# Kernel tuning notes

Measured on AMD Instinct MI355X. Metric: run time of the kernel, lower is better.

Reference implementation:

```python
import jax, jax.numpy as jnp
import numpy as np

N = 14        # nodes per graph (fixed by hidden*14 in the Linear)
H = 4         # attention heads
F_IN = 128    # num_feature
C = 64        # hidden (per-head out_channels; concat=False -> mean over heads)
NEG_SLOPE = 0.2  # PyG GATConv default negative_slope


def gat_conv(x, src, dst, W, a_src, a_dst, b):
    """One PyG-style GATConv on a single graph.
    x: [N, F]  W: [F, H*C]  a_src/a_dst: [H, C]  b: [C]
    src/dst: [E] int (self-loops already appended). concat=False -> mean over heads.
    """
    h = (x @ W).reshape(N, H, C)                       # [N,H,C]
    al_src = jnp.einsum('nhc,hc->nh', h, a_src)        # [N,H]
    al_dst = jnp.einsum('nhc,hc->nh', h, a_dst)        # [N,H]
    e = jax.nn.leaky_relu(al_src[src] + al_dst[dst], NEG_SLOPE)  # [E,H]
    # softmax over incoming edges of each destination node (stable)
    m = jax.ops.segment_max(e, dst, num_segments=N)    # [N,H]
    ex = jnp.exp(e - m[dst])
    denom = jax.ops.segment_sum(ex, dst, num_segments=N)
    alpha = ex / denom[dst]                            # [E,H]
    out = jax.ops.segment_sum(alpha[:, :, None] * h[src], dst, num_segments=N)  # [N,H,C]
    return out.mean(axis=1) + b                        # [N,C]


def setup_inputs() -> dict:
    key = jax.random.key(0)
    ks = jax.random.split(key, 12)
    B, E = 16384, 182
    feature = jax.random.normal(ks[0], (B, N, F_IN), dtype=jnp.float32)
    edge_list = jax.random.randint(ks[1], (B, E, 2), 0, N, dtype=jnp.int64)

    def glorot(k, shape):
        fan = shape[0] + shape[-1]
        return jax.random.normal(k, shape, dtype=jnp.float32) * jnp.sqrt(2.0 / fan)

    return {
        'feature': feature,
        'edge_list': edge_list,
        'W1': glorot(ks[2], (F_IN, H * C)),
        'a_src1': glorot(ks[3], (H, C)),
        'a_dst1': glorot(ks[4], (H, C)),
        'b1': jnp.zeros((C,), jnp.float32),
        'W2': glorot(ks[5], (C, H * C)),
        'a_src2': glorot(ks[6], (H, C)),
        'a_dst2': glorot(ks[7], (H, C)),
        'b2': jnp.zeros((C,), jnp.float32),
        'W_lin': glorot(ks[8], (N * C, C // 2)),
        'b_lin': jnp.zeros((C // 2,), jnp.float32),
        'W_pred': glorot(ks[9], (C // 2, 1)),
        'b_pred': jnp.zeros((1,), jnp.float32),
    }


def reference(feature, edge_list, W1, a_src1, a_dst1, b1, W2, a_src2, a_dst2, b2,
              W_lin, b_lin, W_pred, b_pred):
    B = feature.shape[0]
    # PyG GATConv adds self-loops by default
    loops = jnp.broadcast_to(jnp.arange(N, dtype=edge_list.dtype), (B, N))
    src = jnp.concatenate([edge_list[..., 0], loops], axis=1)  # [B, E+N]
    dst = jnp.concatenate([edge_list[..., 1], loops], axis=1)

    def per_graph(x, s, d):
        h = jax.nn.relu(gat_conv(x, s, d, W1, a_src1, a_dst1, b1))
        # dropout is identity in eval mode
        h = gat_conv(h, s, d, W2, a_src2, a_dst2, b2)       # [N,C]
        z = h.reshape(-1) @ W_lin + b_lin                    # [C//2]
        p = z @ W_pred + b_pred                              # [1]
        return jax.nn.sigmoid(p)

    return jax.vmap(per_graph)(feature, src, dst)            # [B,1]
```

## Files before the change

kernel.cpp:

```cpp
#include <hip/hip_runtime.h>

#define NN 14
#define EE 182

typedef __attribute__((ext_vector_type(8))) short bf16x8;
typedef __attribute__((ext_vector_type(4))) short bf16x4;
typedef __attribute__((ext_vector_type(4))) float f32x4;
typedef __attribute__((ext_vector_type(4))) unsigned u32x4;
typedef __attribute__((ext_vector_type(2))) unsigned u32x2;

__device__ __forceinline__ unsigned f2bf(float f) {
    unsigned u = __float_as_uint(f);
    return (u + 0x7fffu + ((u >> 16) & 1u)) >> 16;
}
__device__ __forceinline__ unsigned pack2bf(float lo, float hi) {
    return __builtin_amdgcn_perm(__float_as_uint(hi) + 0x8000u,
                                 __float_as_uint(lo) + 0x8000u, 0x07060302u);
}
__device__ __forceinline__ bf16x8 mk8(unsigned a, unsigned b, unsigned c, unsigned d) {
    u32x4 u = {a, b, c, d};
    return __builtin_bit_cast(bf16x8, u);
}
__device__ __forceinline__ bf16x4 mk4(unsigned a, unsigned b) {
    u32x2 u = {a, b};
    return __builtin_bit_cast(bf16x4, u);
}

__global__ void prep_pack(const float* __restrict__ W1, const float* __restrict__ W2,
                          const float* __restrict__ Wl, const float* __restrict__ Wpred,
                          const float* __restrict__ bl, const float* __restrict__ bp,
                          const float* __restrict__ as1, const float* __restrict__ ad1,
                          const float* __restrict__ as2, const float* __restrict__ ad2,
                          short* __restrict__ wp1, short* __restrict__ wp2,
                          short* __restrict__ battn1, short* __restrict__ battn2,
                          float* __restrict__ wcombP) {
    int gid = blockIdx.x * 256 + threadIdx.x;
    if (gid < 32768) {
        int j = gid & 7, L = (gid >> 3) & 63, kk = (gid >> 9) & 3, nt = gid >> 11;
        int k = kk * 32 + (L >> 4) * 8 + j, n = nt * 16 + (L & 15);
        wp1[gid] = (short)f2bf(W1[k * 256 + n]);
    } else if (gid < 49152) {
        int g2 = gid - 32768;
        int j = g2 & 7, L = (g2 >> 3) & 63, kk = (g2 >> 9) & 1, nt = g2 >> 10;
        int k = kk * 32 + (L >> 4) * 8 + j, n = nt * 16 + (L & 15);
        wp2[g2] = (short)f2bf(W2[k * 256 + n]);
    } else if (gid < 51200) {
        int g2 = gid - 49152;
        int j = g2 & 7, L = (g2 >> 3) & 63, kk = g2 >> 9;
        int n = L & 15, k = kk * 32 + (L >> 4) * 8 + j;
        float val = 0.f;
        if (n < 8) {
            const float* av = ((n >> 2) ? ad1 : as1) + (n & 3) * 64;
            const float* wr = W1 + k * 256 + (n & 3) * 64;
            for (int c = 0; c < 64; ++c) val += wr[c] * av[c];
        }
        battn1[g2] = (short)f2bf(val);
    } else if (gid < 52224) {
        int g2 = gid - 51200;
        int j = g2 & 7, L = (g2 >> 3) & 63, kk = g2 >> 9;
        int n = L & 15, k = kk * 32 + (L >> 4) * 8 + j;
        float val = 0.f;
        if (n < 8) {
            const float* av = ((n >> 2) ? ad2 : as2) + (n & 3) * 64;
            const float* wr = W2 + k * 256 + (n & 3) * 64;
            for (int c = 0; c < 64; ++c) val += wr[c] * av[c];
        }
        battn2[g2] = (short)f2bf(val);
    } else if (gid < 56320) {
        int o = gid - 52224;
        int r = o & 3, i4 = o >> 2;
        int m = i4 & 15, ctq = i4 >> 4;
        int q = ctq & 3, ct = ctq >> 2;
        int chan = ct * 16 + q * 4 + r;
        float acc = 0.f;
        if (m < NN) {
            const float* wr = Wl + (m * 64 + chan) * 32;
            #pragma unroll
            for (int j = 0; j < 32; ++j) acc += wr[j] * Wpred[j];
        }
        wcombP[o] = acc;
    } else if (gid == 56320) {
        float acc = bp[0];
        #pragma unroll
        for (int j = 0; j < 32; ++j) acc += bl[j] * Wpred[j];
        wcombP[4096] = acc;
    }
}

template<int KK, bool RELU>
__device__ __forceinline__ void gat_layer(int lane,
    const bf16x8* a, const short* wpB,
    const float* __restrict__ bias,
    const float* cntf, const float* alsd,
    f32x4* o, unsigned (*po)[2])
{
    const int m = lane & 15, q = lane >> 4;
    f32x4 agg[4];
    #pragma unroll
    for (int ct = 0; ct < 4; ++ct) agg[ct] = f32x4{0.f, 0.f, 0.f, 0.f};

    #pragma unroll
    for (int h = 0; h < 4; ++h) {
        unsigned hf[4][2];
        #pragma unroll
        for (int ct = 0; ct < 4; ++ct) {
            f32x4 c = f32x4{0.f, 0.f, 0.f, 0.f};
            #pragma unroll
            for (int kk = 0; kk < KK; ++kk) {
                bf16x8 b = *(const bf16x8*)(wpB +
                    (((h * 4 + ct) * KK + kk) * 64 + lane) * 8);
                c = __builtin_amdgcn_mfma_f32_16x16x32_bf16(a[kk], b, c, 0, 0, 0);
            }
            hf[ct][0] = pack2bf(c[0], c[1]);
            hf[ct][1] = pack2bf(c[2], c[3]);
        }

        f32x4 alv = *(const f32x4*)(alsd + h * 16 + q * 4);
        float ad  = alsd[64 + h * 16 + m];
        f32x4 cv  = *(const f32x4*)(cntf + m * 20 + q * 4);
        float v0, v1, v2, v3;
        {
            float l0 = alv[0] + ad, l1 = alv[1] + ad, l2 = alv[2] + ad, l3 = alv[3] + ad;
            l0 = fmaxf(l0, 0.f) + 0.2f * fminf(l0, 0.f);
            l1 = fmaxf(l1, 0.f) + 0.2f * fminf(l1, 0.f);
            l2 = fmaxf(l2, 0.f) + 0.2f * fminf(l2, 0.f);
            l3 = fmaxf(l3, 0.f) + 0.2f * fminf(l3, 0.f);
            v0 = __expf(l0) * cv[0]; v1 = __expf(l1) * cv[1];
            v2 = __expf(l2) * cv[2]; v3 = __expf(l3) * cv[3];
        }
        float s = v0 + v1 + v2 + v3;
        s += __shfl_xor(s, 16);
        s += __shfl_xor(s, 32);
        float inv = (s > 0.f) ? 0.25f / s : 0.f;
        bf16x4 P = mk4(pack2bf(v0 * inv, v1 * inv), pack2bf(v2 * inv, v3 * inv));

        #pragma unroll
        for (int ct = 0; ct < 4; ++ct)
            agg[ct] = __builtin_amdgcn_mfma_f32_16x16x16bf16_1k(
                mk4(hf[ct][0], hf[ct][1]), P, agg[ct], 0, 0, 0);
    }

    #pragma unroll
    for (int ct = 0; ct < 4; ++ct) {
        float4 bb = *(const float4*)(bias + ct * 16 + q * 4);
        float o0 = agg[ct][0] + bb.x, o1 = agg[ct][1] + bb.y;
        float o2 = agg[ct][2] + bb.z, o3 = agg[ct][3] + bb.w;
        if (RELU) {
            o0 = fmaxf(o0, 0.f); o1 = fmaxf(o1, 0.f);
            o2 = fmaxf(o2, 0.f); o3 = fmaxf(o3, 0.f);
            if (m >= NN) { o0 = 0.f; o1 = 0.f; o2 = 0.f; o3 = 0.f; }
            po[ct][0] = pack2bf(o0, o1);
            po[ct][1] = pack2bf(o2, o3);
        } else {
            o[ct] = f32x4{o0, o1, o2, o3};
        }
    }
}

__global__ __launch_bounds__(1024, 4) void gat_fused(
    const float* __restrict__ feature,
    const int*   __restrict__ edge_list,
    const float* __restrict__ b1, const float* __restrict__ b2,
    const short* __restrict__ wpck,
    const float* __restrict__ wcombP,
    float* __restrict__ out, int B)
{
    const int w = threadIdx.x >> 6, lane = threadIdx.x & 63;
    const int m = lane & 15, q = lane >> 4;

    __shared__ __align__(16) short    swts[52224];
    __shared__ __align__(16) unsigned slab[16 * 448];

    float* cntf = (float*)(slab + w * 448);
    float* alsd = (float*)(slab + w * 448 + 320);

    {
        const u32x4* srcw = (const u32x4*)wpck;
        u32x4* dstw = (u32x4*)swts;
        #pragma unroll
        for (int r = 0; r < 7; ++r) {
            int i = r * 1024 + (int)threadIdx.x;
            if (i < 6528) dstw[i] = srcw[i];
        }
    }
    __syncthreads();

    const short* swp1  = swts;
    const short* swp2  = swts + 32768;
    const short* sbat1 = swts + 49152;
    const short* sbat2 = swts + 51200;

    const int g0 = blockIdx.x * 64 + w * 4;

    #pragma clang loop unroll(disable)
    for (int it = 0; it < 4; ++it) {
        const int g = g0 + it;
        if (g >= B) break;

        #pragma unroll
        for (int i = 0; i < 5; ++i) cntf[i * 64 + lane] = 0.f;
        {
            const int2* ep = (const int2*)edge_list + (size_t)g * EE;
            #pragma unroll
            for (int r = 0; r < 3; ++r) {
                int i = r * 64 + lane;
                if (i < EE) { int2 e = ep[i]; atomicAdd(&cntf[e.y * 20 + e.x], 1.f); }
            }
            if (lane < NN) atomicAdd(&cntf[lane * 21], 1.f);
        }

        bf16x8 a1[4];
        #pragma unroll
        for (int kk = 0; kk < 4; ++kk) a1[kk] = mk8(0, 0, 0, 0);
        if (m < NN) {
            const float* xg = feature + (size_t)g * (NN * 128) + m * 128;
            #pragma unroll
            for (int kk = 0; kk < 4; ++kk) {
                float4 v0 = *(const float4*)(xg + kk * 32 + q * 8);
                float4 v1 = *(const float4*)(xg + kk * 32 + q * 8 + 4);
                a1[kk] = mk8(pack2bf(v0.x, v0.y), pack2bf(v0.z, v0.w),
                             pack2bf(v1.x, v1.y), pack2bf(v1.z, v1.w));
            }
        }

        {
            f32x4 ca = f32x4{0.f, 0.f, 0.f, 0.f};
            #pragma unroll
            for (int kk = 0; kk < 4; ++kk) {
                bf16x8 b = *(const bf16x8*)(sbat1 + (kk * 64 + lane) * 8);
                ca = __builtin_amdgcn_mfma_f32_16x16x32_bf16(a1[kk], b, ca, 0, 0, 0);
            }
            if (m < 8) *(f32x4*)(alsd + (m >> 2) * 64 + (m & 3) * 16 + q * 4) = ca;
        }

        unsigned po1[4][2];
        gat_layer<4, true>(lane, a1, swp1, b1, cntf, alsd, nullptr, po1);

        bf16x8 a2[2];
        {
            int ad0 = ((q & 1) * 32 + m) * 4;
            int ad1_ = ad0 + 64;
            bool hi = (q >> 1) != 0;
            #pragma unroll
            for (int kk = 0; kk < 2; ++kk) {
                unsigned sA0 = __builtin_amdgcn_ds_bpermute(ad0, (int)po1[2 * kk][0]);
                unsigned sA1 = __builtin_amdgcn_ds_bpermute(ad0, (int)po1[2 * kk][1]);
                unsigned sB0 = __builtin_amdgcn_ds_bpermute(ad0, (int)po1[2 * kk + 1][0]);
                unsigned sB1 = __builtin_amdgcn_ds_bpermute(ad0, (int)po1[2 * kk + 1][1]);
                unsigned tA0 = __builtin_amdgcn_ds_bpermute(ad1_, (int)po1[2 * kk][0]);
                unsigned tA1 = __builtin_amdgcn_ds_bpermute(ad1_, (int)po1[2 * kk][1]);
                unsigned tB0 = __builtin_amdgcn_ds_bpermute(ad1_, (int)po1[2 * kk + 1][0]);
                unsigned tB1 = __builtin_amdgcn_ds_bpermute(ad1_, (int)po1[2 * kk + 1][1]);
                a2[kk] = mk8(hi ? sB0 : sA0, hi ? sB1 : sA1,
                             hi ? tB0 : tA0, hi ? tB1 : tA1);
            }
        }

        {
            f32x4 ca = f32x4{0.f, 0.f, 0.f, 0.f};
            #pragma unroll
            for (int kk = 0; kk < 2; ++kk) {
                bf16x8 b = *(const bf16x8*)(sbat2 + (kk * 64 + lane) * 8);
                ca = __builtin_amdgcn_mfma_f32_16x16x32_bf16(a2[kk], b, ca, 0, 0, 0);
            }
            if (m < 8) *(f32x4*)(alsd + (m >> 2) * 64 + (m & 3) * 16 + q * 4) = ca;
        }

        f32x4 o2[4];
        gat_layer<2, false>(lane, a2, swp2, b2, cntf, alsd, o2, nullptr);

        float p = 0.f;
        #pragma unroll
        for (int ct = 0; ct < 4; ++ct) {
            float4 wv = *(const float4*)(wcombP + ((ct * 4 + q) * 16 + m) * 4);
            p += o2[ct][0] * wv.x + o2[ct][1] * wv.y +
                 o2[ct][2] * wv.z + o2[ct][3] * wv.w;
        }
        p += __shfl_xor(p, 1);  p += __shfl_xor(p, 2);  p += __shfl_xor(p, 4);
        p += __shfl_xor(p, 8);  p += __shfl_xor(p, 16); p += __shfl_xor(p, 32);
        if (lane == 0) out[g] = 1.f / (1.f + __expf(-(p + wcombP[4096])));
    }
}

extern "C" void kernel_launch(void* const* d_in, const int* in_sizes, int n_in,
                              void* d_out, int out_size, void* d_ws, size_t ws_size,
                              hipStream_t stream) {
    const float* feature = (const float*)d_in[0];
    const int*   edges   = (const int*)d_in[1];
    const float* W1  = (const float*)d_in[2];
    const float* as1 = (const float*)d_in[3];
    const float* ad1 = (const float*)d_in[4];
    const float* b1  = (const float*)d_in[5];
    const float* W2  = (const float*)d_in[6];
    const float* as2 = (const float*)d_in[7];
    const float* ad2 = (const float*)d_in[8];
    const float* b2  = (const float*)d_in[9];
    const float* Wl  = (const float*)d_in[10];
    const float* bl  = (const float*)d_in[11];
    const float* Wp  = (const float*)d_in[12];
    const float* bp  = (const float*)d_in[13];
    float* out = (float*)d_out;

    short* wp1    = (short*)d_ws;
    short* wp2    = wp1 + 32768;
    short* battn1 = wp2 + 16384;
    short* battn2 = battn1 + 2048;
    float* wcombP = (float*)(battn2 + 1024);

    prep_pack<<<221, 256, 0, stream>>>(W1, W2, Wl, Wp, bl, bp, as1, ad1, as2, ad2,
                                       wp1, wp2, battn1, battn2, wcombP);

    const int B = in_sizes[0] / (NN * 128);
    gat_fused<<<(B + 63) / 64, 1024, 0, stream>>>(feature, edges, b1, b2,
                                                  wp1, wcombP, out, B);
}
```

Before: 231.0 us.

## Process two graphs per wave iteration to share weight loads across MFMAs

Each wave now handles two graphs per loop iteration instead of one, interleaving their MFMA chains. Every weight fragment read from LDS is reused for both graphs, and the softmax weights are computed before the projection loop. This halves LDS weight traffic per graph and exposes more independent MFMA work to hide latency. In exchange it doubles per-wave LDS scratch and raises register pressure under launch_bounds(1024,4), which risks spills.

```diff
diff --git a/kernel.cpp b/kernel.cpp
--- a/kernel.cpp
+++ b/kernel.cpp
@@ -88,71 +88,75 @@
 }
 
 template<int KK, bool RELU>
-__device__ __forceinline__ void gat_layer(int lane,
-    const bf16x8* a, const short* wpB,
-    const float* __restrict__ bias,
-    const float* cntf, const float* alsd,
-    f32x4* o, unsigned (*po)[2])
+__device__ __forceinline__ void gat_layer2(int lane,
+    const bf16x8 (*a)[KK], const short* wpB,
+    const float* __restrict__ bias, const float* slabw,
+    f32x4 (*o)[4], unsigned (*po)[4][2])
 {
     const int m = lane & 15, q = lane >> 4;
-    f32x4 agg[4];
+    f32x4 agg[2][4];
     #pragma unroll
-    for (int ct = 0; ct < 4; ++ct) agg[ct] = f32x4{0.f, 0.f, 0.f, 0.f};
+    for (int u = 0; u < 2; ++u)
+        #pragma unroll
+        for (int ct = 0; ct < 4; ++ct) agg[u][ct] = f32x4{0.f, 0.f, 0.f, 0.f};
 
     #pragma unroll
     for (int h = 0; h < 4; ++h) {
-        unsigned hf[4][2];
-        #pragma unroll
-        for (int ct = 0; ct < 4; ++ct) {
-            f32x4 c = f32x4{0.f, 0.f, 0.f, 0.f};
-            #pragma unroll
-            for (int kk = 0; kk < KK; ++kk) {
-                bf16x8 b = *(const bf16x8*)(wpB +
-                    (((h * 4 + ct) * KK + kk) * 64 + lane) * 8);
-                c = __builtin_amdgcn_mfma_f32_16x16x32_bf16(a[kk], b, c, 0, 0, 0);
-            }
-            hf[ct][0] = pack2bf(c[0], c[1]);
-            hf[ct][1] = pack2bf(c[2], c[3]);
-        }
-
-        f32x4 alv = *(const f32x4*)(alsd + h * 16 + q * 4);
-        float ad  = alsd[64 + h * 16 + m];
-        f32x4 cv  = *(const f32x4*)(cntf + m * 20 + q * 4);
-        float v0, v1, v2, v3;
-        {
+        bf16x4 P[2];
+        #pragma unroll
+        for (int u = 0; u < 2; ++u) {
+            const float* cntf = slabw + u * 448;
+            const float* alsd = cntf + 320;
+            f32x4 alv = *(const f32x4*)(alsd + h * 16 + q * 4);
+            float ad  = alsd[64 + h * 16 + m];
+            f32x4 cv  = *(const f32x4*)(cntf + m * 20 + q * 4);
             float l0 = alv[0] + ad, l1 = alv[1] + ad, l2 = alv[2] + ad, l3 = alv[3] + ad;
             l0 = fmaxf(l0, 0.f) + 0.2f * fminf(l0, 0.f);
             l1 = fmaxf(l1, 0.f) + 0.2f * fminf(l1, 0.f);
             l2 = fmaxf(l2, 0.f) + 0.2f * fminf(l2, 0.f);
             l3 = fmaxf(l3, 0.f) + 0.2f * fminf(l3, 0.f);
-            v0 = __expf(l0) * cv[0]; v1 = __expf(l1) * cv[1];
-            v2 = __expf(l2) * cv[2]; v3 = __expf(l3) * cv[3];
-        }
-        float s = v0 + v1 + v2 + v3;
-        s += __shfl_xor(s, 16);
-        s += __shfl_xor(s, 32);
-        float inv = (s > 0.f) ? 0.25f / s : 0.f;
-        bf16x4 P = mk4(pack2bf(v0 * inv, v1 * inv), pack2bf(v2 * inv, v3 * inv));
-
-        #pragma unroll
-        for (int ct = 0; ct < 4; ++ct)
-            agg[ct] = __builtin_amdgcn_mfma_f32_16x16x16bf16_1k(
-                mk4(hf[ct][0], hf[ct][1]), P, agg[ct], 0, 0, 0);
+            float v0 = __expf(l0) * cv[0], v1 = __expf(l1) * cv[1];
+            float v2 = __expf(l2) * cv[2], v3 = __expf(l3) * cv[3];
+            float s = v0 + v1 + v2 + v3;
+            s += __shfl_xor(s, 16);
+            s += __shfl_xor(s, 32);
+            float inv = (s > 0.f) ? 0.25f / s : 0.f;
+            P[u] = mk4(pack2bf(v0 * inv, v1 * inv), pack2bf(v2 * inv, v3 * inv));
+        }
+
+        #pragma unroll
+        for (int ct = 0; ct < 4; ++ct) {
+            f32x4 c0 = f32x4{0.f, 0.f, 0.f, 0.f}, c1 = f32x4{0.f, 0.f, 0.f, 0.f};
+            #pragma unroll
+            for (int kk = 0; kk < KK; ++kk) {
+                bf16x8 b = *(const bf16x8*)(wpB +
+                    (((h * 4 + ct) * KK + kk) * 64 + lane) * 8);
+                c0 = __builtin_amdgcn_mfma_f32_16x16x32_bf16(a[0][kk], b, c0, 0, 0, 0);
+                c1 = __builtin_amdgcn_mfma_f32_16x16x32_bf16(a[1][kk], b, c1, 0, 0, 0);
+            }
+            agg[0][ct] = __builtin_amdgcn_mfma_f32_16x16x16bf16_1k(
+                mk4(pack2bf(c0[0], c0[1]), pack2bf(c0[2], c0[3])), P[0], agg[0][ct], 0, 0, 0);
+            agg[1][ct] = __builtin_amdgcn_mfma_f32_16x16x16bf16_1k(
+                mk4(pack2bf(c1[0], c1[1]), pack2bf(c1[2], c1[3])), P[1], agg[1][ct], 0, 0, 0);
+        }
     }
 
     #pragma unroll
     for (int ct = 0; ct < 4; ++ct) {
         float4 bb = *(const float4*)(bias + ct * 16 + q * 4);
-        float o0 = agg[ct][0] + bb.x, o1 = agg[ct][1] + bb.y;
-        float o2 = agg[ct][2] + bb.z, o3 = agg[ct][3] + bb.w;
-        if (RELU) {
-            o0 = fmaxf(o0, 0.f); o1 = fmaxf(o1, 0.f);
-            o2 = fmaxf(o2, 0.f); o3 = fmaxf(o3, 0.f);
-            if (m >= NN) { o0 = 0.f; o1 = 0.f; o2 = 0.f; o3 = 0.f; }
-            po[ct][0] = pack2bf(o0, o1);
-            po[ct][1] = pack2bf(o2, o3);
-        } else {
-            o[ct] = f32x4{o0, o1, o2, o3};
+        #pragma unroll
+        for (int u = 0; u < 2; ++u) {
+            float o0 = agg[u][ct][0] + bb.x, o1 = agg[u][ct][1] + bb.y;
+            float o2v = agg[u][ct][2] + bb.z, o3 = agg[u][ct][3] + bb.w;
+            if (RELU) {
+                o0 = fmaxf(o0, 0.f);  o1 = fmaxf(o1, 0.f);
+                o2v = fmaxf(o2v, 0.f); o3 = fmaxf(o3, 0.f);
+                if (m >= NN) { o0 = 0.f; o1 = 0.f; o2v = 0.f; o3 = 0.f; }
+                po[u][ct][0] = pack2bf(o0, o1);
+                po[u][ct][1] = pack2bf(o2v, o3);
+            } else {
+                o[u][ct] = f32x4{o0, o1, o2v, o3};
+            }
         }
     }
 }
@@ -169,10 +173,9 @@
     const int m = lane & 15, q = lane >> 4;
 
     __shared__ __align__(16) short    swts[52224];
-    __shared__ __align__(16) unsigned slab[16 * 448];
-
-    float* cntf = (float*)(slab + w * 448);
-    float* alsd = (float*)(slab + w * 448 + 320);
+    __shared__ __align__(16) unsigned slab[16 * 896];
+
+    float* slabw = (float*)(slab + w * 896);
 
     {
         const u32x4* srcw = (const u32x4*)wpck;
@@ -193,92 +196,140 @@
     const int g0 = blockIdx.x * 64 + w * 4;
 
     #pragma clang loop unroll(disable)
-    for (int it = 0; it < 4; ++it) {
-        const int g = g0 + it;
+    for (int it = 0; it < 2; ++it) {
+        const int g = g0 + it * 2;
         if (g >= B) break;
-
-        #pragma unroll
-        for (int i = 0; i < 5; ++i) cntf[i * 64 + lane] = 0.f;
+        const bool act1 = (g + 1) < B;
+        float* cnt0 = slabw;
+        float* cnt1 = slabw + 448;
+
+        #pragma unroll
+        for (int i = 0; i < 5; ++i) {
+            cnt0[i * 64 + lane] = 0.f;
+            cnt1[i * 64 + lane] = 0.f;
+        }
         {
-            const int2* ep = (const int2*)edge_list + (size_t)g * EE;
+            const int2* ep0 = (const int2*)edge_list + (size_t)g * EE;
+            const int2* ep1 = ep0 + EE;
             #pragma unroll
             for (int r = 0; r < 3; ++r) {
                 int i = r * 64 + lane;
-                if (i < EE) { int2 e = ep[i]; atomicAdd(&cntf[e.y * 20 + e.x], 1.f); }
-            }
-            if (lane < NN) atomicAdd(&cntf[lane * 21], 1.f);
-        }
-
-        bf16x8 a1[4];
-        #pragma unroll
-        for (int kk = 0; kk < 4; ++kk) a1[kk] = mk8(0, 0, 0, 0);
+                if (i < EE) {
+                    int2 e0 = ep0[i];
+                    atomicAdd(&cnt0[e0.y * 20 + e0.x], 1.f);
+                    if (act1) { int2 e1 = ep1[i]; atomicAdd(&cnt1[e1.y * 20 + e1.x], 1.f); }
+                }
+            }
+            if (lane < NN) {
+                atomicAdd(&cnt0[lane * 21], 1.f);
+                if (act1) atomicAdd(&cnt1[lane * 21], 1.f);
+            }
+        }
+
+        bf16x8 a1[2][4];
+        #pragma unroll
+        for (int u = 0; u < 2; ++u)
+            #pragma unroll
+            for (int kk = 0; kk < 4; ++kk) a1[u][kk] = mk8(0, 0, 0, 0);
         if (m < NN) {
-            const float* xg = feature + (size_t)g * (NN * 128) + m * 128;
+            const float* xg0 = feature + (size_t)g * (NN * 128) + m * 128;
             #pragma unroll
             for (int kk = 0; kk < 4; ++kk) {
-                float4 v0 = *(const float4*)(xg + kk * 32 + q * 8);
-                float4 v1 = *(const float4*)(xg + kk * 32 + q * 8 + 4);
-                a1[kk] = mk8(pack2bf(v0.x, v0.y), pack2bf(v0.z, v0.w),
-                             pack2bf(v1.x, v1.y), pack2bf(v1.z, v1.w));
+                float4 v0 = *(const float4*)(xg0 + kk * 32 + q * 8);
+                float4 v1 = *(const float4*)(xg0 + kk * 32 + q * 8 + 4);
+                a1[0][kk] = mk8(pack2bf(v0.x, v0.y), pack2bf(v0.z, v0.w),
+                                pack2bf(v1.x, v1.y), pack2bf(v1.z, v1.w));
+            }
+        }
+        if (act1 && m < NN) {
+            const float* xg1 = feature + (size_t)(g + 1) * (NN * 128) + m * 128;
+            #pragma unroll
+            for (int kk = 0; kk < 4; ++kk) {
+                float4 v0 = *(const float4*)(xg1 + kk * 32 + q * 8);
+                float4 v1 = *(const float4*)(xg1 + kk * 32 + q * 8 + 4);
+                a1[1][kk] = mk8(pack2bf(v0.x, v0.y), pack2bf(v0.z, v0.w),
+                                pack2bf(v1.x, v1.y), pack2bf(v1.z, v1.w));
             }
         }
 
         {
-            f32x4 ca = f32x4{0.f, 0.f, 0.f, 0.f};
+            f32x4 ca0 = f32x4{0.f, 0.f, 0.f, 0.f}, ca1 = f32x4{0.f, 0.f, 0.f, 0.f};
             #pragma unroll
             for (int kk = 0; kk < 4; ++kk) {
                 bf16x8 b = *(const bf16x8*)(sbat1 + (kk * 64 + lane) * 8);
-                ca = __builtin_amdgcn_mfma_f32_16x16x32_bf16(a1[kk], b, ca, 0, 0, 0);
-            }
-            if (m < 8) *(f32x4*)(alsd + (m >> 2) * 64 + (m & 3) * 16 + q * 4) = ca;
-        }
-
-        unsigned po1[4][2];
-        gat_layer<4, true>(lane, a1, swp1, b1, cntf, alsd, nullptr, po1);
-
-        bf16x8 a2[2];
+                ca0 = __builtin_amdgcn_mfma_f32_16x16x32_bf16(a1[0][kk], b, ca0, 0, 0, 0);
+                ca1 = __builtin_amdgcn_mfma_f32_16x16x32_bf16(a1[1][kk], b, ca1, 0, 0, 0);
+            }
+            if (m < 8) {
+                int off = (m >> 2) * 64 + (m & 3) * 16 + q * 4;
+                *(f32x4*)(slabw + 320 + off) = ca0;
+                *(f32x4*)(slabw + 448 + 320 + off) = ca1;
+            }
+        }
+
+        unsigned po1[2][4][2];
+        gat_layer2<4, true>(lane, a1, swp1, b1, slabw, nullptr, po1);
+
+        bf16x8 a2[2][2];
         {
             int ad0 = ((q & 1) * 32 + m) * 4;
             int ad1_ = ad0 + 64;
             bool hi = (q >> 1) != 0;
             #pragma unroll
+            for (int u = 0; u < 2; ++u)
+            #pragma unroll
             for (int kk = 0; kk < 2; ++kk) {
-                unsigned sA0 = __builtin_amdgcn_ds_bpermute(ad0, (int)po1[2 * kk][0]);
-                unsigned sA1 = __builtin_amdgcn_ds_bpermute(ad0, (int)po1[2 * kk][1]);
-                unsigned sB0 = __builtin_amdgcn_ds_bpermute(ad0, (int)po1[2 * kk + 1][0]);
-                unsigned sB1 = __builtin_amdgcn_ds_bpermute(ad0, (int)po1[2 * kk + 1][1]);
-                unsigned tA0 = __builtin_amdgcn_ds_bpermute(ad1_, (int)po1[2 * kk][0]);
-                unsigned tA1 = __builtin_amdgcn_ds_bpermute(ad1_, (int)po1[2 * kk][1]);
-                unsigned tB0 = __builtin_amdgcn_ds_bpermute(ad1_, (int)po1[2 * kk + 1][0]);
-                unsigned tB1 = __builtin_amdgcn_ds_bpermute(ad1_, (int)po1[2 * kk + 1][1]);
-                a2[kk] = mk8(hi ? sB0 : sA0, hi ? sB1 : sA1,
-                             hi ? tB0 : tA0, hi ? tB1 : tA1);
+                unsigned sA0 = __builtin_amdgcn_ds_bpermute(ad0, (int)po1[u][2 * kk][0]);
+                unsigned sA1 = __builtin_amdgcn_ds_bpermute(ad0, (int)po1[u][2 * kk][1]);
+                unsigned sB0 = __builtin_amdgcn_ds_bpermute(ad0, (int)po1[u][2 * kk + 1][0]);
+                unsigned sB1 = __builtin_amdgcn_ds_bpermute(ad0, (int)po1[u][2 * kk + 1][1]);
+                unsigned tA0 = __builtin_amdgcn_ds_bpermute(ad1_, (int)po1[u][2 * kk][0]);
+                unsigned tA1 = __builtin_amdgcn_ds_bpermute(ad1_, (int)po1[u][2 * kk][1]);
+                unsigned tB0 = __builtin_amdgcn_ds_bpermute(ad1_, (int)po1[u][2 * kk + 1][0]);
+                unsigned tB1 = __builtin_amdgcn_ds_bpermute(ad1_, (int)po1[u][2 * kk + 1][1]);
+                a2[u][kk] = mk8(hi ? sB0 : sA0, hi ? sB1 : sA1,
+                                hi ? tB0 : tA0, hi ? tB1 : tA1);
             }
         }
 
         {
-            f32x4 ca = f32x4{0.f, 0.f, 0.f, 0.f};
+            f32x4 ca0 = f32x4{0.f, 0.f, 0.f, 0.f}, ca1 = f32x4{0.f, 0.f, 0.f, 0.f};
             #pragma unroll
             for (int kk = 0; kk < 2; ++kk) {
                 bf16x8 b = *(const bf16x8*)(sbat2 + (kk * 64 + lane) * 8);
-                ca = __builtin_amdgcn_mfma_f32_16x16x32_bf16(a2[kk], b, ca, 0, 0, 0);
-            }
-            if (m < 8) *(f32x4*)(alsd + (m >> 2) * 64 + (m & 3) * 16 + q * 4) = ca;
-        }
-
-        f32x4 o2[4];
-        gat_layer<2, false>(lane, a2, swp2, b2, cntf, alsd, o2, nullptr);
-
-        float p = 0.f;
+                ca0 = __builtin_amdgcn_mfma_f32_16x16x32_bf16(a2[0][kk], b, ca0, 0, 0, 0);
+                ca1 = __builtin_amdgcn_mfma_f32_16x16x32_bf16(a2[1][kk], b, ca1, 0, 0, 0);
+            }
+            if (m < 8) {
+                int off = (m >> 2) * 64 + (m & 3) * 16 + q * 4;
+                *(f32x4*)(slabw + 320 + off) = ca0;
+                *(f32x4*)(slabw + 448 + 320 + off) = ca1;
+            }
+        }
+
+        f32x4 o2[2][4];
+        gat_layer2<2, false>(lane, a2, swp2, b2, slabw, o2, nullptr);
+
+        float p0 = 0.f, p1 = 0.f;
         #pragma unroll
         for (int ct = 0; ct < 4; ++ct) {
             float4 wv = *(const float4*)(wcombP + ((ct * 4 + q) * 16 + m) * 4);
-            p += o2[ct][0] * wv.x + o2[ct][1] * wv.y +
-                 o2[ct][2] * wv.z + o2[ct][3] * wv.w;
-        }
-        p += __shfl_xor(p, 1);  p += __shfl_xor(p, 2);  p += __shfl_xor(p, 4);
-        p += __shfl_xor(p, 8);  p += __shfl_xor(p, 16); p += __shfl_xor(p, 32);
-        if (lane == 0) out[g] = 1.f / (1.f + __expf(-(p + wcombP[4096])));
+            p0 += o2[0][ct][0] * wv.x + o2[0][ct][1] * wv.y +
+                  o2[0][ct][2] * wv.z + o2[0][ct][3] * wv.w;
+            p1 += o2[1][ct][0] * wv.x + o2[1][ct][1] * wv.y +
+                  o2[1][ct][2] * wv.z + o2[1][ct][3] * wv.w;
+        }
+        p0 += __shfl_xor(p0, 1);  p1 += __shfl_xor(p1, 1);
+        p0 += __shfl_xor(p0, 2);  p1 += __shfl_xor(p1, 2);
+        p0 += __shfl_xor(p0, 4);  p1 += __shfl_xor(p1, 4);
+        p0 += __shfl_xor(p0, 8);  p1 += __shfl_xor(p1, 8);
+        p0 += __shfl_xor(p0, 16); p1 += __shfl_xor(p1, 16);
+        p0 += __shfl_xor(p0, 32); p1 += __shfl_xor(p1, 32);
+        if (lane == 0) {
+            float cc = wcombP[4096];
+            out[g] = 1.f / (1.f + __expf(-(p0 + cc)));
+            if (act1) out[g + 1] = 1.f / (1.f + __expf(-(p1 + cc)));
+        }
     }
 }
 
```

New measurement: 234.1 us. No clear change (+1.4%).

## Shrink blocks to one graph per wave, read layer-1 weights from global, byte edge counts

Applied to the files above, without the earlier changes.

Each block now has 8 waves with one graph per wave instead of 16 waves looping over 4 graphs. Layer-1 packed weights are read directly from global/L2 rather than staged in LDS. Only layer-2 and attention weights go to LDS, and edge counts are stored as packed bytes updated with integer atomics. Attention probabilities for all heads are computed before the MFMA loop so projection and aggregation interleave per tile. The goal is lower LDS use and higher occupancy, at the cost of more global weight traffic and more per-block staging overhead from the extra blocks.

```diff
diff --git a/kernel.cpp b/kernel.cpp
--- a/kernel.cpp
+++ b/kernel.cpp
@@ -88,20 +88,42 @@
 }
 
 template<int KK, bool RELU>
-__device__ __forceinline__ void gat_layer(int lane,
+__device__ __forceinline__ void gat_layer1g(int lane,
     const bf16x8* a, const short* wpB,
     const float* __restrict__ bias,
-    const float* cntf, const float* alsd,
+    const unsigned char* cnt, const float* alsd,
     f32x4* o, unsigned (*po)[2])
 {
     const int m = lane & 15, q = lane >> 4;
+
+    bf16x4 P[4];
+    #pragma unroll
+    for (int h = 0; h < 4; ++h) {
+        f32x4 alv = *(const f32x4*)(alsd + h * 16 + q * 4);
+        float ad  = alsd[64 + h * 16 + m];
+        unsigned cw = *(const unsigned*)(cnt + m * 20 + q * 4);
+        float l0 = alv[0] + ad, l1 = alv[1] + ad, l2 = alv[2] + ad, l3 = alv[3] + ad;
+        l0 = fmaxf(l0, 0.f) + 0.2f * fminf(l0, 0.f);
+        l1 = fmaxf(l1, 0.f) + 0.2f * fminf(l1, 0.f);
+        l2 = fmaxf(l2, 0.f) + 0.2f * fminf(l2, 0.f);
+        l3 = fmaxf(l3, 0.f) + 0.2f * fminf(l3, 0.f);
+        float v0 = __expf(l0) * (float)(cw & 255u);
+        float v1 = __expf(l1) * (float)((cw >> 8) & 255u);
+        float v2 = __expf(l2) * (float)((cw >> 16) & 255u);
+        float v3 = __expf(l3) * (float)(cw >> 24);
+        float s = v0 + v1 + v2 + v3;
+        s += __shfl_xor(s, 16);
+        s += __shfl_xor(s, 32);
+        float inv = (s > 0.f) ? 0.25f / s : 0.f;
+        P[h] = mk4(pack2bf(v0 * inv, v1 * inv), pack2bf(v2 * inv, v3 * inv));
+    }
+
     f32x4 agg[4];
     #pragma unroll
     for (int ct = 0; ct < 4; ++ct) agg[ct] = f32x4{0.f, 0.f, 0.f, 0.f};
 
     #pragma unroll
     for (int h = 0; h < 4; ++h) {
-        unsigned hf[4][2];
         #pragma unroll
         for (int ct = 0; ct < 4; ++ct) {
             f32x4 c = f32x4{0.f, 0.f, 0.f, 0.f};
@@ -111,175 +133,159 @@
                     (((h * 4 + ct) * KK + kk) * 64 + lane) * 8);
                 c = __builtin_amdgcn_mfma_f32_16x16x32_bf16(a[kk], b, c, 0, 0, 0);
             }
-            hf[ct][0] = pack2bf(c[0], c[1]);
-            hf[ct][1] = pack2bf(c[2], c[3]);
-        }
-
-        f32x4 alv = *(const f32x4*)(alsd + h * 16 + q * 4);
-        float ad  = alsd[64 + h * 16 + m];
-        f32x4 cv  = *(const f32x4*)(cntf + m * 20 + q * 4);
-        float v0, v1, v2, v3;
-        {
-            float l0 = alv[0] + ad, l1 = alv[1] + ad, l2 = alv[2] + ad, l3 = alv[3] + ad;
-            l0 = fmaxf(l0, 0.f) + 0.2f * fminf(l0, 0.f);
-            l1 = fmaxf(l1, 0.f) + 0.2f * fminf(l1, 0.f);
-            l2 = fmaxf(l2, 0.f) + 0.2f * fminf(l2, 0.f);
-            l3 = fmaxf(l3, 0.f) + 0.2f * fminf(l3, 0.f);
-            v0 = __expf(l0) * cv[0]; v1 = __expf(l1) * cv[1];
-            v2 = __expf(l2) * cv[2]; v3 = __expf(l3) * cv[3];
-        }
-        float s = v0 + v1 + v2 + v3;
-        s += __shfl_xor(s, 16);
-        s += __shfl_xor(s, 32);
-        float inv = (s > 0.f) ? 0.25f / s : 0.f;
-        bf16x4 P = mk4(pack2bf(v0 * inv, v1 * inv), pack2bf(v2 * inv, v3 * inv));
-
-        #pragma unroll
-        for (int ct = 0; ct < 4; ++ct)
             agg[ct] = __builtin_amdgcn_mfma_f32_16x16x16bf16_1k(
-                mk4(hf[ct][0], hf[ct][1]), P, agg[ct], 0, 0, 0);
+                mk4(pack2bf(c[0], c[1]), pack2bf(c[2], c[3])), P[h], agg[ct], 0, 0, 0);
+        }
     }
 
     #pragma unroll
     for (int ct = 0; ct < 4; ++ct) {
         float4 bb = *(const float4*)(bias + ct * 16 + q * 4);
         float o0 = agg[ct][0] + bb.x, o1 = agg[ct][1] + bb.y;
-        float o2 = agg[ct][2] + bb.z, o3 = agg[ct][3] + bb.w;
+        float o2v = agg[ct][2] + bb.z, o3 = agg[ct][3] + bb.w;
         if (RELU) {
-            o0 = fmaxf(o0, 0.f); o1 = fmaxf(o1, 0.f);
-            o2 = fmaxf(o2, 0.f); o3 = fmaxf(o3, 0.f);
-            if (m >= NN) { o0 = 0.f; o1 = 0.f; o2 = 0.f; o3 = 0.f; }
+            o0 = fmaxf(o0, 0.f);  o1 = fmaxf(o1, 0.f);
+            o2v = fmaxf(o2v, 0.f); o3 = fmaxf(o3, 0.f);
+            if (m >= NN) { o0 = 0.f; o1 = 0.f; o2v = 0.f; o3 = 0.f; }
             po[ct][0] = pack2bf(o0, o1);
-            po[ct][1] = pack2bf(o2, o3);
+            po[ct][1] = pack2bf(o2v, o3);
         } else {
-            o[ct] = f32x4{o0, o1, o2, o3};
-        }
-    }
-}
-
-__global__ __launch_bounds__(1024, 4) void gat_fused(
+            o[ct] = f32x4{o0, o1, o2v, o3};
+        }
+    }
+}
+
+__global__ __launch_bounds__(512)
+__attribute__((amdgpu_waves_per_eu(6)))
+void gat_fused(
     const float* __restrict__ feature,
     const int*   __restrict__ edge_list,
     const float* __restrict__ b1, const float* __restrict__ b2,
-    const short* __restrict__ wpck,
+    const short* __restrict__ wp1g,
+    const short* __restrict__ wpck2,
     const float* __restrict__ wcombP,
     float* __restrict__ out, int B)
 {
     const int w = threadIdx.x >> 6, lane = threadIdx.x & 63;
     const int m = lane & 15, q = lane >> 4;
 
-    __shared__ __align__(16) short    swts[52224];
-    __shared__ __align__(16) unsigned slab[16 * 448];
-
-    float* cntf = (float*)(slab + w * 448);
-    float* alsd = (float*)(slab + w * 448 + 320);
-
-    {
-        const u32x4* srcw = (const u32x4*)wpck;
+    __shared__ __align__(16) short    swts[19456];
+    __shared__ __align__(16) unsigned slab[8 * 208];
+
+    unsigned* swave = slab + w * 208;
+    unsigned char* cnt = (unsigned char*)swave;
+    float* alsd = (float*)(swave + 80);
+
+    {
+        const u32x4* srcw = (const u32x4*)wpck2;
         u32x4* dstw = (u32x4*)swts;
         #pragma unroll
-        for (int r = 0; r < 7; ++r) {
-            int i = r * 1024 + (int)threadIdx.x;
-            if (i < 6528) dstw[i] = srcw[i];
+        for (int r = 0; r < 5; ++r) {
+            int i = r * 512 + (int)threadIdx.x;
+            if (i < 2432) dstw[i] = srcw[i];
         }
     }
     __syncthreads();
 
-    const short* swp1  = swts;
-    const short* swp2  = swts + 32768;
-    const short* sbat1 = swts + 49152;
-    const short* sbat2 = swts + 51200;
-
-    const int g0 = blockIdx.x * 64 + w * 4;
-
-    #pragma clang loop unroll(disable)
-    for (int it = 0; it < 4; ++it) {
-        const int g = g0 + it;
-        if (g >= B) break;
-
-        #pragma unroll
-        for (int i = 0; i < 5; ++i) cntf[i * 64 + lane] = 0.f;
-        {
-            const int2* ep = (const int2*)edge_list + (size_t)g * EE;
-            #pragma unroll
-            for (int r = 0; r < 3; ++r) {
-                int i = r * 64 + lane;
-                if (i < EE) { int2 e = ep[i]; atomicAdd(&cntf[e.y * 20 + e.x], 1.f); }
+    const short* swp2  = swts;
+    const short* sbat1 = swts + 16384;
+    const short* sbat2 = swts + 18432;
+
+    const int g = blockIdx.x * 8 + w;
+    if (g >= B) return;
+
+    {
+        if (lane < 64) swave[lane] = 0u;
+        if (lane < 16) swave[64 + lane] = 0u;
+        const int2* ep = (const int2*)edge_list + (size_t)g * EE;
+        #pragma unroll
+        for (int r = 0; r < 3; ++r) {
+            int i = r * 64 + lane;
+            if (i < EE) {
+                int2 e = ep[i];
+                int b = e.y * 20 + e.x;
+                atomicAdd((unsigned*)(cnt + (b & ~3)), 1u << ((b & 3) * 8));
             }
-            if (lane < NN) atomicAdd(&cntf[lane * 21], 1.f);
-        }
-
-        bf16x8 a1[4];
+        }
+        if (lane < NN) {
+            int b = lane * 21;
+            atomicAdd((unsigned*)(cnt + (b & ~3)), 1u << ((b & 3) * 8));
+        }
+    }
+
+    bf16x8 a1[4];
+    if (m < NN) {
+        const float* xg = feature + (size_t)g * (NN * 128) + m * 128;
+        #pragma unroll
+        for (int kk = 0; kk < 4; ++kk) {
+            float4 v0 = *(const float4*)(xg + kk * 32 + q * 8);
+            float4 v1 = *(const float4*)(xg + kk * 32 + q * 8 + 4);
+            a1[kk] = mk8(pack2bf(v0.x, v0.y), pack2bf(v0.z, v0.w),
+                         pack2bf(v1.x, v1.y), pack2bf(v1.z, v1.w));
+        }
+    } else {
         #pragma unroll
         for (int kk = 0; kk < 4; ++kk) a1[kk] = mk8(0, 0, 0, 0);
-        if (m < NN) {
-            const float* xg = feature + (size_t)g * (NN * 128) + m * 128;
-            #pragma unroll
-            for (int kk = 0; kk < 4; ++kk) {
-                float4 v0 = *(const float4*)(xg + kk * 32 + q * 8);
-                float4 v1 = *(const float4*)(xg + kk * 32 + q * 8 + 4);
-                a1[kk] = mk8(pack2bf(v0.x, v0.y), pack2bf(v0.z, v0.w),
-                             pack2bf(v1.x, v1.y), pack2bf(v1.z, v1.w));
-            }
-        }
-
-        {
-            f32x4 ca = f32x4{0.f, 0.f, 0.f, 0.f};
-            #pragma unroll
-            for (int kk = 0; kk < 4; ++kk) {
-                bf16x8 b = *(const bf16x8*)(sbat1 + (kk * 64 + lane) * 8);
-                ca = __builtin_amdgcn_mfma_f32_16x16x32_bf16(a1[kk], b, ca, 0, 0, 0);
-            }
-            if (m < 8) *(f32x4*)(alsd + (m >> 2) * 64 + (m & 3) * 16 + q * 4) = ca;
-        }
-
-        unsigned po1[4][2];
-        gat_layer<4, true>(lane, a1, swp1, b1, cntf, alsd, nullptr, po1);
-
-        bf16x8 a2[2];
-        {
-            int ad0 = ((q & 1) * 32 + m) * 4;
-            int ad1_ = ad0 + 64;
-            bool hi = (q >> 1) != 0;
-            #pragma unroll
-            for (int kk = 0; kk < 2; ++kk) {
-                unsigned sA0 = __builtin_amdgcn_ds_bpermute(ad0, (int)po1[2 * kk][0]);
-                unsigned sA1 = __builtin_amdgcn_ds_bpermute(ad0, (int)po1[2 * kk][1]);
-                unsigned sB0 = __builtin_amdgcn_ds_bpermute(ad0, (int)po1[2 * kk + 1][0]);
-                unsigned sB1 = __builtin_amdgcn_ds_bpermute(ad0, (int)po1[2 * kk + 1][1]);
-                unsigned tA0 = __builtin_amdgcn_ds_bpermute(ad1_, (int)po1[2 * kk][0]);
-                unsigned tA1 = __builtin_amdgcn_ds_bpermute(ad1_, (int)po1[2 * kk][1]);
-                unsigned tB0 = __builtin_amdgcn_ds_bpermute(ad1_, (int)po1[2 * kk + 1][0]);
-                unsigned tB1 = __builtin_amdgcn_ds_bpermute(ad1_, (int)po1[2 * kk + 1][1]);
-                a2[kk] = mk8(hi ? sB0 : sA0, hi ? sB1 : sA1,
-                             hi ? tB0 : tA0, hi ? tB1 : tA1);
-            }
-        }
-
-        {
-            f32x4 ca = f32x4{0.f, 0.f, 0.f, 0.f};
-            #pragma unroll
-            for (int kk = 0; kk < 2; ++kk) {
-                bf16x8 b = *(const bf16x8*)(sbat2 + (kk * 64 + lane) * 8);
-                ca = __builtin_amdgcn_mfma_f32_16x16x32_bf16(a2[kk], b, ca, 0, 0, 0);
-            }
-            if (m < 8) *(f32x4*)(alsd + (m >> 2) * 64 + (m & 3) * 16 + q * 4) = ca;
-        }
-
-        f32x4 o2[4];
-        gat_layer<2, false>(lane, a2, swp2, b2, cntf, alsd, o2, nullptr);
-
-        float p = 0.f;
-        #pragma unroll
-        for (int ct = 0; ct < 4; ++ct) {
-            float4 wv = *(const float4*)(wcombP + ((ct * 4 + q) * 16 + m) * 4);
-            p += o2[ct][0] * wv.x + o2[ct][1] * wv.y +
-                 o2[ct][2] * wv.z + o2[ct][3] * wv.w;
-        }
-        p += __shfl_xor(p, 1);  p += __shfl_xor(p, 2);  p += __shfl_xor(p, 4);
-        p += __shfl_xor(p, 8);  p += __shfl_xor(p, 16); p += __shfl_xor(p, 32);
-        if (lane == 0) out[g] = 1.f / (1.f + __expf(-(p + wcombP[4096])));
-    }
+    }
+
+    {
+        f32x4 ca = f32x4{0.f, 0.f, 0.f, 0.f};
+        #pragma unroll
+        for (int kk = 0; kk < 4; ++kk) {
+            bf16x8 b = *(const bf16x8*)(sbat1 + (kk * 64 + lane) * 8);
+            ca = __builtin_amdgcn_mfma_f32_16x16x32_bf16(a1[kk], b, ca, 0, 0, 0);
+        }
+        if (m < 8)
+            *(f32x4*)(alsd + (m >> 2) * 64 + (m & 3) * 16 + q * 4) = ca;
+    }
+
+    unsigned po1[4][2];
+    gat_layer1g<4, true>(lane, a1, wp1g, b1, cnt, alsd, nullptr, po1);
+
+    bf16x8 a2[2];
+    {
+        int ad0 = ((q & 1) * 32 + m) * 4;
+        int ad1_ = ad0 + 64;
+        bool hi = (q >> 1) != 0;
+        #pragma unroll
+        for (int kk = 0; kk < 2; ++kk) {
+            unsigned sA0 = __builtin_amdgcn_ds_bpermute(ad0, (int)po1[2 * kk][0]);
+            unsigned sA1 = __builtin_amdgcn_ds_bpermute(ad0, (int)po1[2 * kk][1]);
+            unsigned sB0 = __builtin_amdgcn_ds_bpermute(ad0, (int)po1[2 * kk + 1][0]);
+            unsigned sB1 = __builtin_amdgcn_ds_bpermute(ad0, (int)po1[2 * kk + 1][1]);
+            unsigned tA0 = __builtin_amdgcn_ds_bpermute(ad1_, (int)po1[2 * kk][0]);
+            unsigned tA1 = __builtin_amdgcn_ds_bpermute(ad1_, (int)po1[2 * kk][1]);
+            unsigned tB0 = __builtin_amdgcn_ds_bpermute(ad1_, (int)po1[2 * kk + 1][0]);
+            unsigned tB1 = __builtin_amdgcn_ds_bpermute(ad1_, (int)po1[2 * kk + 1][1]);
+            a2[kk] = mk8(hi ? sB0 : sA0, hi ? sB1 : sA1,
+                         hi ? tB0 : tA0, hi ? tB1 : tA1);
+        }
+    }
+
+    {
+        f32x4 ca = f32x4{0.f, 0.f, 0.f, 0.f};
+        #pragma unroll
+        for (int kk = 0; kk < 2; ++kk) {
+            bf16x8 b = *(const bf16x8*)(sbat2 + (kk * 64 + lane) * 8);
+            ca = __builtin_amdgcn_mfma_f32_16x16x32_bf16(a2[kk], b, ca, 0, 0, 0);
+        }
+        if (m < 8)
+            *(f32x4*)(alsd + (m >> 2) * 64 + (m & 3) * 16 + q * 4) = ca;
+    }
+
+    f32x4 o2[4];
+    gat_layer1g<2, false>(lane, a2, swp2, b2, cnt, alsd, o2, nullptr);
+
+    float p = 0.f;
+    #pragma unroll
+    for (int ct = 0; ct < 4; ++ct) {
+        float4 wv = *(const float4*)(wcombP + ((ct * 4 + q) * 16 + m) * 4);
+        p += o2[ct][0] * wv.x + o2[ct][1] * wv.y +
+             o2[ct][2] * wv.z + o2[ct][3] * wv.w;
+    }
+    p += __shfl_xor(p, 1);  p += __shfl_xor(p, 2);  p += __shfl_xor(p, 4);
+    p += __shfl_xor(p, 8);  p += __shfl_xor(p, 16); p += __shfl_xor(p, 32);
+    if (lane == 0) out[g] = 1.f / (1.f + __expf(-(p + wcombP[4096])));
 }
 
 extern "C" void kernel_launch(void* const* d_in, const int* in_sizes, int n_in,
@@ -311,6 +317,6 @@
                                        wp1, wp2, battn1, battn2, wcombP);
 
     const int B = in_sizes[0] / (NN * 128);
-    gat_fused<<<(B + 63) / 64, 1024, 0, stream>>>(feature, edges, b1, b2,
-                                                  wp1, wcombP, out, B);
-}
+    gat_fused<<<(B + 7) / 8, 512, 0, stream>>>(feature, edges, b1, b2,
+                                               wp1, wp2, wcombP, out, B);
+}
```

After: 254.9 us. +10.3%, slower.
